# Optimization experiments

Measured on AMD Instinct MI355X. Metric: run time of the kernel, lower is better.

Reference implementation:

```python
import jax, jax.numpy as jnp
import numpy as np

N, E, D, ED = 50000, 800000, 64, 2


def setup_inputs() -> dict:
    key = jax.random.key(0)
    ks = jax.random.split(key, 16)
    inp = {
        "h": jax.random.normal(ks[0], (N, D), jnp.float32),
        "coord": jax.random.normal(ks[1], (N, 3), jnp.float32),
        "edge_index": jax.random.randint(ks[2], (2, E), 0, N, jnp.int32),
        "edge_attr": jax.random.normal(ks[3], (E, ED), jnp.float32),
        # edge_mlp: Linear(2D+1+ED -> D), Linear(D -> D)
        "W_e1": jax.random.normal(ks[4], (2 * D + 1 + ED, D), jnp.float32) * 0.08,
        "b_e1": jnp.zeros((D,), jnp.float32),
        "W_e2": jax.random.normal(ks[5], (D, D), jnp.float32) * 0.12,
        "b_e2": jnp.zeros((D,), jnp.float32),
        # node_mlp: Linear(D+D -> D), Linear(D -> D)
        "W_n1": jax.random.normal(ks[6], (2 * D, D), jnp.float32) * 0.08,
        "b_n1": jnp.zeros((D,), jnp.float32),
        "W_n2": jax.random.normal(ks[7], (D, D), jnp.float32) * 0.12,
        "b_n2": jnp.zeros((D,), jnp.float32),
        # coord_mlp: Linear(D -> D), Linear(D -> 1, bias=False, xavier gain 0.001)
        "W_c1": jax.random.normal(ks[8], (D, D), jnp.float32) * 0.12,
        "b_c1": jnp.zeros((D,), jnp.float32),
        "W_c2": jax.random.normal(ks[9], (D, 1), jnp.float32) * 1e-3,
    }
    return inp


def reference(h, coord, edge_index, edge_attr,
              W_e1, b_e1, W_e2, b_e2,
              W_n1, b_n1, W_n2, b_n2,
              W_c1, b_c1, W_c2):
    row, col = edge_index[0], edge_index[1]
    n_nodes = h.shape[0]

    # coord2radial
    coord_diff = coord[row] - coord[col]                       # [E,3]
    radial = jnp.sum(coord_diff * coord_diff, axis=-1, keepdims=True)  # [E,1]

    # edge_model
    e_in = jnp.concatenate([h[row], h[col], radial, edge_attr], axis=-1)  # [E, 2D+1+ED]
    e = jax.nn.silu(e_in @ W_e1 + b_e1)
    edge_feat = jax.nn.silu(e @ W_e2 + b_e2)                   # [E,D]

    # coord_model: trans = coord_diff * coord_mlp(edge_feat), clamp, segment mean
    scale = jax.nn.silu(edge_feat @ W_c1 + b_c1) @ W_c2        # [E,1]
    trans = jnp.clip(coord_diff * scale, -100.0, 100.0)        # [E,3]
    agg_c = jax.ops.segment_sum(trans, row, num_segments=n_nodes)       # [N,3]
    cnt = jax.ops.segment_sum(jnp.ones((trans.shape[0],), trans.dtype), row,
                              num_segments=n_nodes)            # [N]
    coord_out = coord + agg_c / jnp.clip(cnt, 1.0, None)[:, None]  # coords_weight=1.0

    # node_model: segment sum of edge_feat by row, node MLP, residual
    agg_h = jax.ops.segment_sum(edge_feat, row, num_segments=n_nodes)   # [N,D]
    n_in = jnp.concatenate([h, agg_h], axis=-1)                # [N,2D]
    h_out = h + (jax.nn.silu(n_in @ W_n1 + b_n1) @ W_n2 + b_n2)

    return (h_out, coord_out)
```

## Files before the change

### kernel.cpp

```cpp
#include <hip/hip_runtime.h>

#define DD 64
#define NTE 512
#define SLOTMAX 64

using s8v   = __attribute__((ext_vector_type(8))) short;
using f32x4 = __attribute__((ext_vector_type(4))) float;

typedef unsigned int   uint_t;
typedef unsigned short ushort_t;

union U8 { s8v v; uint_t u[4]; };

__device__ __forceinline__ float silu_f(float x) {
    return x / (1.0f + __expf(-x));
}
__device__ __forceinline__ float clamp100(float x) {
    return fminf(fmaxf(x, -100.0f), 100.0f);
}
__device__ __forceinline__ unsigned short f2bf(float x) {
    unsigned int u = __float_as_uint(x);
    return (unsigned short)((u + 0x7FFFu + ((u >> 16) & 1u)) >> 16);
}
__device__ __forceinline__ uint_t cvt_pk_bf16(float lo, float hi) {
    uint_t r;
    asm("v_cvt_pk_bf16_f32 %0, %1, %2" : "=v"(r) : "v"(lo), "v"(hi));
    return r;
}

#define WAVE_FENCE() do { asm volatile("s_waitcnt lgkmcnt(0)" ::: "memory"); \
                          __builtin_amdgcn_sched_barrier(0); } while (0)

__global__ __launch_bounds__(256) void prep_all(
    const float* __restrict__ h,
    const float* __restrict__ We1, const float* __restrict__ We2,
    const float* __restrict__ Wc1,
    const float* __restrict__ Wn1, const float* __restrict__ Wn2,
    const float* __restrict__ be1, const float* __restrict__ be2,
    const float* __restrict__ bc1,
    const int*   __restrict__ ei,
    ushort_t* __restrict__ hbf,
    ushort_t* __restrict__ wf,
    int* __restrict__ cnt_i,
    int* __restrict__ slots,
    int E, int total8, int histBlocks, int hbfBlocks)
{
    const int b = blockIdx.x;
    if (b < histBlocks) {
        const int e = b * 256 + threadIdx.x;
        if (e < E) {
            const int r = ei[e];
            const int s = atomicAdd(&cnt_i[r], 1);
            if (s < SLOTMAX) slots[(size_t)r * SLOTMAX + s] = e;
        }
    } else if (b < histBlocks + hbfBlocks) {
        const int t = (b - histBlocks) * 256 + threadIdx.x;
        if (t < total8) {
            const float4 v0 = ((const float4*)h)[t * 2 + 0];
            const float4 v1 = ((const float4*)h)[t * 2 + 1];
            uint4 o;
            o.x = (uint_t)f2bf(v0.x) | ((uint_t)f2bf(v0.y) << 16);
            o.y = (uint_t)f2bf(v0.z) | ((uint_t)f2bf(v0.w) << 16);
            o.z = (uint_t)f2bf(v1.x) | ((uint_t)f2bf(v1.y) << 16);
            o.w = (uint_t)f2bf(v1.z) | ((uint_t)f2bf(v1.w) << 16);
            ((uint4*)hbf)[t] = o;
        }
    } else {
        const int t = (b - histBlocks - hbfBlocks) * 256 + threadIdx.x;
        if (t >= 32768) return;
        if (t < 28672) {
            const int j    = t & 7;
            const int lane = (t >> 3) & 63;
            const int n0   = (t >> 9) & 3;
            const int k0   = (t >> 11) & 1;
            const int mat  = t >> 12;
            const int g    = lane >> 4;
            int k;
            if (mat == 2 || mat == 3) k = 16 * (2 * k0 + (j >> 2)) + 4 * g + (j & 3);
            else                      k = k0 * 32 + g * 8 + j;
            const int n = n0 * 16 + (lane & 15);
            float v;
            if      (mat == 0) v = We1[(size_t)k * 64 + n];
            else if (mat == 1) v = We1[(size_t)(64 + k) * 64 + n];
            else if (mat == 2) v = We2[(size_t)k * 64 + n];
            else if (mat == 3) v = Wc1[(size_t)k * 64 + n];
            else if (mat == 4) v = Wn1[(size_t)k * 64 + n];
            else if (mat == 5) v = Wn1[(size_t)(64 + k) * 64 + n];
            else               v = Wn2[(size_t)k * 64 + n];
            wf[t] = f2bf(v);
        } else {
            const int t2   = t - 28672;
            const int j    = t2 & 7;
            const int lane = (t2 >> 3) & 63;
            const int n0   = (t2 >> 9) & 3;
            const int xm   = (t2 >> 11) & 1;
            const int k = 8 * (lane >> 4) + j;
            const int m = n0 * 16 + (lane & 15);
            float v = 0.0f;
            if (xm == 0) {
                if      (k == 0) v = We1[(size_t)128 * 64 + m];
                else if (k == 1) v = We1[(size_t)129 * 64 + m];
                else if (k == 2) v = We1[(size_t)130 * 64 + m];
                else if (k == 3) v = be1[m];
            } else {
                if      (k == 0) v = be2[m];
                else if (k == 1) v = bc1[m];
            }
            wf[t] = f2bf(v);
        }
    }
}

__global__ __launch_bounds__(NTE, 4) void egcl_edge(
    const ushort_t* __restrict__ hbf,
    const ushort_t* __restrict__ wfG,
    const float* __restrict__ coord,
    const int*   __restrict__ ei,
    const float* __restrict__ ea,
    const float* __restrict__ Wc2,
    const int* __restrict__ cnt_i,
    const int* __restrict__ slots,
    ushort_t* __restrict__ aggbf,
    float* __restrict__ coord_out,
    int N, int E, int totalWaves)
{
    __shared__ ushort_t fragLDS[20480];

    const int tid = threadIdx.x;
    #pragma unroll
    for (int i = 0; i < 4; ++i)
        ((uint4*)fragLDS)[tid + i * 512] = ((const uint4*)wfG)[tid + i * 512];
    ((uint4*)fragLDS)[2048 + tid] = ((const uint4*)wfG)[3584 + tid];
    __syncthreads();

    const int wid  = tid >> 6;
    const int lane = tid & 63;
    const int l15  = lane & 15;
    const int g    = lane >> 4;

#define LD_W(mat, k0, m0) \
    (*(const s8v*)(fragLDS + ((((mat)*2 + (k0))*4 + (m0)) * 512) + lane * 8))
#define LD_X7(m0) (*(const s8v*)(fragLDS + 16384 + (m0) * 512 + lane * 8))
#define LD_XB(m0) (*(const s8v*)(fragLDS + 18432 + (m0) * 512 + lane * 8))

    float wc2_c[4][4];
    #pragma unroll
    for (int m0 = 0; m0 < 4; ++m0)
        #pragma unroll
        for (int j = 0; j < 4; ++j)
            wc2_c[m0][j] = Wc2[m0 * 16 + 4 * g + j];

    U8 b2f, bcf;
    b2f.u[0] = 0x00003F80u; b2f.u[1] = 0; b2f.u[2] = 0; b2f.u[3] = 0;
    bcf.u[0] = 0x3F800000u; bcf.u[1] = 0; bcf.u[2] = 0; bcf.u[3] = 0;

    const f32x4 zero4 = {0.f, 0.f, 0.f, 0.f};

    int n = blockIdx.x * 8 + wid;
    int pdeg = 0, pslot = 0;
    if (n < N) {
        pdeg  = cnt_i[n];
        pslot = slots[(size_t)n * SLOTMAX + l15];
    }

    for (; n < N; n += totalWaves) {
        const int deg   = pdeg;
        const int slot0 = pslot;
        const int nn = n + totalWaves;
        if (nn < N) {
            pdeg  = cnt_i[nn];
            pslot = slots[(size_t)nn * SLOTMAX + l15];
        }

        const int effdeg = deg < SLOTMAX ? deg : SLOTMAX;
        const float cnx = coord[n * 3 + 0];
        const float cny = coord[n * 3 + 1];
        const float cnz = coord[n * 3 + 2];
        const int slot0_l0 = __shfl(slot0, lane & 48, 64);

        const ushort_t* hn = hbf + (size_t)n * 64;
        const s8v bn0 = *(const s8v*)(hn + g * 8);
        const s8v bn1 = *(const s8v*)(hn + 32 + g * 8);
        f32x4 rowacc[4];
        #pragma unroll
        for (int m0 = 0; m0 < 4; ++m0) {
            f32x4 a = zero4;
            a = __builtin_amdgcn_mfma_f32_16x16x32_bf16(LD_W(0, 0, m0), bn0, a, 0, 0, 0);
            a = __builtin_amdgcn_mfma_f32_16x16x32_bf16(LD_W(0, 1, m0), bn1, a, 0, 0, 0);
            rowacc[m0] = a;
        }

        float hsum[4][4];
        #pragma unroll
        for (int m0 = 0; m0 < 4; ++m0)
            #pragma unroll
            for (int j = 0; j < 4; ++j) hsum[m0][j] = 0.f;
        float txs = 0.f, tys = 0.f, tzs = 0.f;

        const int ntile = (effdeg + 15) >> 4;
        for (int t = 0; t < ntile; ++t) {
            const int s = t * 16 + l15;
            const bool val = (s < effdeg);
            int eL;
            if (t == 0) eL = val ? slot0 : slot0_l0;
            else        eL = slots[(size_t)n * SLOTMAX + (val ? s : 0)];

            const int ci = ei[E + eL];
            const float cx = coord[ci * 3 + 0];
            const float cy = coord[ci * 3 + 1];
            const float cz = coord[ci * 3 + 2];
            const float dx = cnx - cx, dy = cny - cy, dz = cnz - cz;
            const float radial = dx * dx + dy * dy + dz * dz;
            const float2 a2 = *(const float2*)(ea + (size_t)eL * 2);
            const ushort_t* hc = hbf + (size_t)ci * 64;
            const s8v bc0 = *(const s8v*)(hc + g * 8);
            const s8v bc1v = *(const s8v*)(hc + 32 + g * 8);

            U8 ex;
            ex.u[0] = cvt_pk_bf16(radial, a2.x);
            ex.u[1] = cvt_pk_bf16(a2.y, 1.0f);
            ex.u[2] = 0; ex.u[3] = 0;

            f32x4 c1[4];
            #pragma unroll
            for (int m0 = 0; m0 < 4; ++m0) {
                f32x4 a = rowacc[m0];
                a = __builtin_amdgcn_mfma_f32_16x16x32_bf16(LD_W(1, 0, m0), bc0,  a, 0, 0, 0);
                a = __builtin_amdgcn_mfma_f32_16x16x32_bf16(LD_W(1, 1, m0), bc1v, a, 0, 0, 0);
                a = __builtin_amdgcn_mfma_f32_16x16x32_bf16(LD_X7(m0),      ex.v, a, 0, 0, 0);
                c1[m0] = a;
            }

            U8 f2a, f2b;
            #pragma unroll
            for (int m0 = 0; m0 < 4; ++m0) {
                const float ya = silu_f(c1[m0][0]);
                const float yb = silu_f(c1[m0][1]);
                const float yc = silu_f(c1[m0][2]);
                const float yd = silu_f(c1[m0][3]);
                U8& dst = (m0 < 2) ? f2a : f2b;
                dst.u[(m0 & 1) * 2 + 0] = cvt_pk_bf16(ya, yb);
                dst.u[(m0 & 1) * 2 + 1] = cvt_pk_bf16(yc, yd);
            }

            f32x4 c2[4];
            #pragma unroll
            for (int m0 = 0; m0 < 4; ++m0) {
                f32x4 a = zero4;
                a = __builtin_amdgcn_mfma_f32_16x16x32_bf16(LD_W(2, 0, m0), f2a.v, a, 0, 0, 0);
                a = __builtin_amdgcn_mfma_f32_16x16x32_bf16(LD_W(2, 1, m0), f2b.v, a, 0, 0, 0);
                a = __builtin_amdgcn_mfma_f32_16x16x32_bf16(LD_XB(m0),      b2f.v, a, 0, 0, 0);
                c2[m0] = a;
            }

            U8 f3a, f3b;
            #pragma unroll
            for (int m0 = 0; m0 < 4; ++m0) {
                const float ya = silu_f(c2[m0][0]);
                const float yb = silu_f(c2[m0][1]);
                const float yc = silu_f(c2[m0][2]);
                const float yd = silu_f(c2[m0][3]);
                hsum[m0][0] += val ? ya : 0.f;
                hsum[m0][1] += val ? yb : 0.f;
                hsum[m0][2] += val ? yc : 0.f;
                hsum[m0][3] += val ? yd : 0.f;
                U8& dst = (m0 < 2) ? f3a : f3b;
                dst.u[(m0 & 1) * 2 + 0] = cvt_pk_bf16(ya, yb);
                dst.u[(m0 & 1) * 2 + 1] = cvt_pk_bf16(yc, yd);
            }

            float p = 0.f;
            #pragma unroll
            for (int m0 = 0; m0 < 4; ++m0) {
                f32x4 a = zero4;
                a = __builtin_amdgcn_mfma_f32_16x16x32_bf16(LD_W(3, 0, m0), f3a.v, a, 0, 0, 0);
                a = __builtin_amdgcn_mfma_f32_16x16x32_bf16(LD_W(3, 1, m0), f3b.v, a, 0, 0, 0);
                a = __builtin_amdgcn_mfma_f32_16x16x32_bf16(LD_XB(m0),      bcf.v, a, 0, 0, 0);
                #pragma unroll
                for (int j = 0; j < 4; ++j)
                    p = fmaf(silu_f(a[j]), wc2_c[m0][j], p);
            }
            p += __shfl_xor(p, 16, 64);
            p += __shfl_xor(p, 32, 64);
            const float sc = val ? p : 0.f;
            txs += clamp100(dx * sc);
            tys += clamp100(dy * sc);
            tzs += clamp100(dz * sc);
        }

        #pragma unroll
        for (int m0 = 0; m0 < 4; ++m0) {
            #pragma unroll
            for (int j = 0; j < 4; ++j) {
                float v = hsum[m0][j];
                v += __shfl_xor(v, 1, 64);
                v += __shfl_xor(v, 2, 64);
                v += __shfl_xor(v, 4, 64);
                v += __shfl_xor(v, 8, 64);
                hsum[m0][j] = v;
            }
        }
        if (l15 == 0) {
            uint_t* ab = (uint_t*)aggbf + (size_t)n * 32 + 2 * g;
            #pragma unroll
            for (int m0 = 0; m0 < 4; ++m0) {
                ab[8 * m0 + 0] = cvt_pk_bf16(hsum[m0][0], hsum[m0][1]);
                ab[8 * m0 + 1] = cvt_pk_bf16(hsum[m0][2], hsum[m0][3]);
            }
        }
        #pragma unroll
        for (int msk = 1; msk < 64; msk <<= 1) {
            txs += __shfl_xor(txs, msk, 64);
            tys += __shfl_xor(tys, msk, 64);
            tzs += __shfl_xor(tzs, msk, 64);
        }
        if (lane == 0) {
            const float inv = 0.25f / fmaxf((float)deg, 1.0f);
            coord_out[(size_t)n * 3 + 0] = cnx + txs * inv;
            coord_out[(size_t)n * 3 + 1] = cny + tys * inv;
            coord_out[(size_t)n * 3 + 2] = cnz + tzs * inv;
        }
    }
#undef LD_W
#undef LD_X7
#undef LD_XB
}

__global__ __launch_bounds__(NTE, 4) void egcl_node(
    const ushort_t* __restrict__ hbf,
    const ushort_t* __restrict__ aggbf,
    const ushort_t* __restrict__ wfG,
    const float* __restrict__ h,
    const float* __restrict__ bn1,
    const float* __restrict__ bn2,
    float* __restrict__ h_out,
    int N)
{
    __shared__ ushort_t fragLDS[12288];
    __shared__ ushort_t ldsY[8][16 * 72];

    const int tid = threadIdx.x;
    #pragma unroll
    for (int i = 0; i < 3; ++i)
        ((uint4*)fragLDS)[tid + i * 512] = ((const uint4*)(wfG + 16384))[tid + i * 512];
    __syncthreads();

    const int wid  = tid >> 6;
    const int lane = tid & 63;
    const int l15  = lane & 15;
    const int g    = lane >> 4;

#define LD_WN(mat, k0, n0) \
    (*(const s8v*)(fragLDS + ((((mat)*2 + (k0))*4 + (n0)) * 512) + lane * 8))

    float bn1_c[4], bn2_c[4];
    #pragma unroll
    for (int n0 = 0; n0 < 4; ++n0) {
        bn1_c[n0] = bn1[n0 * 16 + l15];
        bn2_c[n0] = bn2[n0 * 16 + l15];
    }

    const int wg = blockIdx.x * 8 + wid;
    const int nb = wg * 16;
    if (nb >= N) return;

    const int nod  = nb + l15;
    const int nodL = nod < N ? nod : N - 1;
    const ushort_t* hrow = hbf   + (size_t)nodL * 64;
    const ushort_t* arow = aggbf + (size_t)nodL * 64;
    const s8v aH0 = *(const s8v*)(hrow + g * 8);
    const s8v aH1 = *(const s8v*)(hrow + 32 + g * 8);
    const s8v aG0 = *(const s8v*)(arow + g * 8);
    const s8v aG1 = *(const s8v*)(arow + 32 + g * 8);

    ushort_t* yw = ldsY[wid];
    #pragma unroll
    for (int n0 = 0; n0 < 4; ++n0) {
        f32x4 a = {0.f, 0.f, 0.f, 0.f};
        a = __builtin_amdgcn_mfma_f32_16x16x32_bf16(aH0, LD_WN(0, 0, n0), a, 0, 0, 0);
        a = __builtin_amdgcn_mfma_f32_16x16x32_bf16(aH1, LD_WN(0, 1, n0), a, 0, 0, 0);
        a = __builtin_amdgcn_mfma_f32_16x16x32_bf16(aG0, LD_WN(1, 0, n0), a, 0, 0, 0);
        a = __builtin_amdgcn_mfma_f32_16x16x32_bf16(aG1, LD_WN(1, 1, n0), a, 0, 0, 0);
        #pragma unroll
        for (int jj = 0; jj < 4; ++jj)
            yw[(g * 4 + jj) * 72 + n0 * 16 + l15] = f2bf(silu_f(a[jj] + bn1_c[n0]));
    }
    WAVE_FENCE();

    const ushort_t* yrow = yw + l15 * 72;
    const s8v b0 = *(const s8v*)(yrow + g * 8);
    const s8v b1 = *(const s8v*)(yrow + 32 + g * 8);
    #pragma unroll
    for (int n0 = 0; n0 < 4; ++n0) {
        f32x4 a = {0.f, 0.f, 0.f, 0.f};
        a = __builtin_amdgcn_mfma_f32_16x16x32_bf16(b0, LD_WN(2, 0, n0), a, 0, 0, 0);
        a = __builtin_amdgcn_mfma_f32_16x16x32_bf16(b1, LD_WN(2, 1, n0), a, 0, 0, 0);
        #pragma unroll
        for (int jj = 0; jj < 4; ++jj) {
            const int m = nb + g * 4 + jj;
            if (m < N) {
                const size_t idx = (size_t)m * 64 + n0 * 16 + l15;
                h_out[idx] = h[idx] + (a[jj] + bn2_c[n0]);
            }
        }
    }
#undef LD_WN
}

extern "C" void kernel_launch(void* const* d_in, const int* in_sizes, int n_in,
                              void* d_out, int out_size, void* d_ws, size_t ws_size,
                              hipStream_t stream) {
    const float* h     = (const float*)d_in[0];
    const float* coord = (const float*)d_in[1];
    const int*   ei    = (const int*)  d_in[2];
    const float* ea    = (const float*)d_in[3];
    const float* We1   = (const float*)d_in[4];
    const float* be1   = (const float*)d_in[5];
    const float* We2   = (const float*)d_in[6];
    const float* be2   = (const float*)d_in[7];
    const float* Wn1   = (const float*)d_in[8];
    const float* bn1   = (const float*)d_in[9];
    const float* Wn2   = (const float*)d_in[10];
    const float* bn2   = (const float*)d_in[11];
    const float* Wc1   = (const float*)d_in[12];
    const float* bc1   = (const float*)d_in[13];
    const float* Wc2   = (const float*)d_in[14];

    const int N = in_sizes[0] / DD;
    const int E = in_sizes[3] / 2;

    float* out       = (float*)d_out;
    float* h_out     = out;
    float* coord_out = out + (size_t)N * DD;

    char* base = (char*)d_ws;
    ushort_t* hbf   = (ushort_t*)base;
    const size_t o_wf    = (size_t)N * DD * 2;
    ushort_t* wf    = (ushort_t*)(base + o_wf);
    const size_t o_agg   = o_wf + 32768 * 2;
    ushort_t* aggbf = (ushort_t*)(base + o_agg);
    const size_t o_cnt   = o_agg + (size_t)N * DD * 2;
    int* cnt_i      = (int*)(base + o_cnt);
    const size_t o_slots = o_cnt + (size_t)N * 4;
    int* slots      = (int*)(base + o_slots);

    hipMemsetAsync((void*)cnt_i, 0, (size_t)N * 4, stream);

    const int histBlocks = (E + 255) / 256;
    const int total8     = N * DD / 8;
    const int hbfBlocks  = (total8 + 255) / 256;
    const int wfBlocks   = (32768 + 255) / 256;
    prep_all<<<histBlocks + hbfBlocks + wfBlocks, 256, 0, stream>>>(
        h, We1, We2, Wc1, Wn1, Wn2, be1, be2, bc1, ei,
        hbf, wf, cnt_i, slots, E, total8, histBlocks, hbfBlocks);

    const int eblocks = 512;
    const int totalWaves = eblocks * 8;
    egcl_edge<<<eblocks, NTE, 0, stream>>>(
        hbf, wf, coord, ei, ea, Wc2,
        cnt_i, slots, aggbf, coord_out, N, E, totalWaves);

    const int nwaves  = (N + 15) / 16;
    const int nblocks = (nwaves + 7) / 8;
    egcl_node<<<nblocks, NTE, 0, stream>>>(
        hbf, aggbf, wf, h, bn1, bn2, h_out, N);
}
```

Baseline: 250.4 us.

## Store column index in slots, pad coords to float4, prefetch next slot tile

The histogram pass now stores (edge id, column node) pairs, so the edge kernel no longer needs a dependent load of edge_index to find the neighbour. Coordinates are repacked into padded float4 so each neighbour's position comes from one vector load. The next tile's slot entries are prefetched inside the loop, and the edge kernel's launch bounds and grid size are doubled to raise occupancy. The cost is a larger slots buffer, an extra prep pass, and tighter register limits under the new launch bounds, which could cause spills.

```diff
diff --git a/kernel.cpp b/kernel.cpp
--- a/kernel.cpp
+++ b/kernel.cpp
@@ -33,6 +33,7 @@
 
 __global__ __launch_bounds__(256) void prep_all(
     const float* __restrict__ h,
+    const float* __restrict__ coord,
     const float* __restrict__ We1, const float* __restrict__ We2,
     const float* __restrict__ Wc1,
     const float* __restrict__ Wn1, const float* __restrict__ Wn2,
@@ -41,9 +42,10 @@
     const int*   __restrict__ ei,
     ushort_t* __restrict__ hbf,
     ushort_t* __restrict__ wf,
+    float4* __restrict__ coord4,
     int* __restrict__ cnt_i,
-    int* __restrict__ slots,
-    int E, int total8, int histBlocks, int hbfBlocks)
+    int2* __restrict__ slots2,
+    int N, int E, int total8, int histBlocks, int hbfBlocks, int c4Blocks)
 {
     const int b = blockIdx.x;
     if (b < histBlocks) {
@@ -51,7 +53,10 @@
         if (e < E) {
             const int r = ei[e];
             const int s = atomicAdd(&cnt_i[r], 1);
-            if (s < SLOTMAX) slots[(size_t)r * SLOTMAX + s] = e;
+            if (s < SLOTMAX) {
+                int2 v; v.x = e; v.y = ei[E + e];
+                slots2[(size_t)r * SLOTMAX + s] = v;
+            }
         }
     } else if (b < histBlocks + hbfBlocks) {
         const int t = (b - histBlocks) * 256 + threadIdx.x;
@@ -65,8 +70,18 @@
             o.w = (uint_t)f2bf(v1.z) | ((uint_t)f2bf(v1.w) << 16);
             ((uint4*)hbf)[t] = o;
         }
+    } else if (b < histBlocks + hbfBlocks + c4Blocks) {
+        const int t = (b - histBlocks - hbfBlocks) * 256 + threadIdx.x;
+        if (t < N) {
+            float4 c;
+            c.x = coord[3 * t + 0];
+            c.y = coord[3 * t + 1];
+            c.z = coord[3 * t + 2];
+            c.w = 0.0f;
+            coord4[t] = c;
+        }
     } else {
-        const int t = (b - histBlocks - hbfBlocks) * 256 + threadIdx.x;
+        const int t = (b - histBlocks - hbfBlocks - c4Blocks) * 256 + threadIdx.x;
         if (t >= 32768) return;
         if (t < 28672) {
             const int j    = t & 7;
@@ -111,18 +126,17 @@
     }
 }
 
-__global__ __launch_bounds__(NTE, 4) void egcl_edge(
+__global__ __launch_bounds__(NTE, 8) void egcl_edge(
     const ushort_t* __restrict__ hbf,
     const ushort_t* __restrict__ wfG,
-    const float* __restrict__ coord,
-    const int*   __restrict__ ei,
+    const float4* __restrict__ coord4,
     const float* __restrict__ ea,
     const float* __restrict__ Wc2,
     const int* __restrict__ cnt_i,
-    const int* __restrict__ slots,
+    const int2* __restrict__ slots2,
     ushort_t* __restrict__ aggbf,
     float* __restrict__ coord_out,
-    int N, int E, int totalWaves)
+    int N, int totalWaves)
 {
     __shared__ ushort_t fragLDS[20480];
 
@@ -157,26 +171,26 @@
     const f32x4 zero4 = {0.f, 0.f, 0.f, 0.f};
 
     int n = blockIdx.x * 8 + wid;
-    int pdeg = 0, pslot = 0;
+    int pdeg = 0;
+    int2 pslot; pslot.x = 0; pslot.y = 0;
     if (n < N) {
         pdeg  = cnt_i[n];
-        pslot = slots[(size_t)n * SLOTMAX + l15];
+        pslot = slots2[(size_t)n * SLOTMAX + l15];
     }
 
     for (; n < N; n += totalWaves) {
-        const int deg   = pdeg;
-        const int slot0 = pslot;
+        const int deg    = pdeg;
+        const int2 slot0 = pslot;
         const int nn = n + totalWaves;
         if (nn < N) {
             pdeg  = cnt_i[nn];
-            pslot = slots[(size_t)nn * SLOTMAX + l15];
+            pslot = slots2[(size_t)nn * SLOTMAX + l15];
         }
 
         const int effdeg = deg < SLOTMAX ? deg : SLOTMAX;
-        const float cnx = coord[n * 3 + 0];
-        const float cny = coord[n * 3 + 1];
-        const float cnz = coord[n * 3 + 2];
-        const int slot0_l0 = __shfl(slot0, lane & 48, 64);
+        const float4 cn4 = coord4[n];
+        const int s0x = __shfl(slot0.x, lane & 48, 64);
+        const int s0y = __shfl(slot0.y, lane & 48, 64);
 
         const ushort_t* hn = hbf + (size_t)n * 64;
         const s8v bn0 = *(const s8v*)(hn + g * 8);
@@ -198,23 +212,30 @@
         float txs = 0.f, tys = 0.f, tzs = 0.f;
 
         const int ntile = (effdeg + 15) >> 4;
+        int2 slNext; slNext.x = 0; slNext.y = 0;
+
         for (int t = 0; t < ntile; ++t) {
             const int s = t * 16 + l15;
             const bool val = (s < effdeg);
-            int eL;
-            if (t == 0) eL = val ? slot0 : slot0_l0;
-            else        eL = slots[(size_t)n * SLOTMAX + (val ? s : 0)];
-
-            const int ci = ei[E + eL];
-            const float cx = coord[ci * 3 + 0];
-            const float cy = coord[ci * 3 + 1];
-            const float cz = coord[ci * 3 + 2];
-            const float dx = cnx - cx, dy = cny - cy, dz = cnz - cz;
+            const float valf = val ? 1.0f : 0.0f;
+
+            int2 sl;
+            if (t == 0) { sl.x = val ? slot0.x : s0x; sl.y = val ? slot0.y : s0y; }
+            else        sl = slNext;
+
+            if (t + 1 < ntile) {
+                const int s2 = s + 16;
+                slNext = slots2[(size_t)n * SLOTMAX + (s2 < effdeg ? s2 : 0)];
+            }
+
+            const float4 c4 = coord4[sl.y];
+            const float2 a2 = *(const float2*)(ea + 2 * (size_t)sl.x);
+            const ushort_t* hc = hbf + (size_t)sl.y * 64;
+            const s8v bc0  = *(const s8v*)(hc + g * 8);
+            const s8v bc1v = *(const s8v*)(hc + 32 + g * 8);
+
+            const float dx = cn4.x - c4.x, dy = cn4.y - c4.y, dz = cn4.z - c4.z;
             const float radial = dx * dx + dy * dy + dz * dz;
-            const float2 a2 = *(const float2*)(ea + (size_t)eL * 2);
-            const ushort_t* hc = hbf + (size_t)ci * 64;
-            const s8v bc0 = *(const s8v*)(hc + g * 8);
-            const s8v bc1v = *(const s8v*)(hc + 32 + g * 8);
 
             U8 ex;
             ex.u[0] = cvt_pk_bf16(radial, a2.x);
@@ -260,10 +281,10 @@
                 const float yb = silu_f(c2[m0][1]);
                 const float yc = silu_f(c2[m0][2]);
                 const float yd = silu_f(c2[m0][3]);
-                hsum[m0][0] += val ? ya : 0.f;
-                hsum[m0][1] += val ? yb : 0.f;
-                hsum[m0][2] += val ? yc : 0.f;
-                hsum[m0][3] += val ? yd : 0.f;
+                hsum[m0][0] = fmaf(ya, valf, hsum[m0][0]);
+                hsum[m0][1] = fmaf(yb, valf, hsum[m0][1]);
+                hsum[m0][2] = fmaf(yc, valf, hsum[m0][2]);
+                hsum[m0][3] = fmaf(yd, valf, hsum[m0][3]);
                 U8& dst = (m0 < 2) ? f3a : f3b;
                 dst.u[(m0 & 1) * 2 + 0] = cvt_pk_bf16(ya, yb);
                 dst.u[(m0 & 1) * 2 + 1] = cvt_pk_bf16(yc, yd);
@@ -282,7 +303,7 @@
             }
             p += __shfl_xor(p, 16, 64);
             p += __shfl_xor(p, 32, 64);
-            const float sc = val ? p : 0.f;
+            const float sc = p * valf;
             txs += clamp100(dx * sc);
             tys += clamp100(dy * sc);
             tzs += clamp100(dz * sc);
@@ -316,9 +337,9 @@
         }
         if (lane == 0) {
             const float inv = 0.25f / fmaxf((float)deg, 1.0f);
-            coord_out[(size_t)n * 3 + 0] = cnx + txs * inv;
-            coord_out[(size_t)n * 3 + 1] = cny + tys * inv;
-            coord_out[(size_t)n * 3 + 2] = cnz + tzs * inv;
+            coord_out[(size_t)n * 3 + 0] = cn4.x + txs * inv;
+            coord_out[(size_t)n * 3 + 1] = cn4.y + tys * inv;
+            coord_out[(size_t)n * 3 + 2] = cn4.z + tzs * inv;
         }
     }
 #undef LD_W
@@ -439,26 +460,30 @@
     ushort_t* wf    = (ushort_t*)(base + o_wf);
     const size_t o_agg   = o_wf + 32768 * 2;
     ushort_t* aggbf = (ushort_t*)(base + o_agg);
-    const size_t o_cnt   = o_agg + (size_t)N * DD * 2;
+    const size_t o_c4    = o_agg + (size_t)N * DD * 2;
+    float4* coord4  = (float4*)(base + o_c4);
+    const size_t o_cnt   = o_c4 + (size_t)N * 16;
     int* cnt_i      = (int*)(base + o_cnt);
     const size_t o_slots = o_cnt + (size_t)N * 4;
-    int* slots      = (int*)(base + o_slots);
+    int2* slots2    = (int2*)(base + o_slots);
 
     hipMemsetAsync((void*)cnt_i, 0, (size_t)N * 4, stream);
 
     const int histBlocks = (E + 255) / 256;
     const int total8     = N * DD / 8;
     const int hbfBlocks  = (total8 + 255) / 256;
+    const int c4Blocks   = (N + 255) / 256;
     const int wfBlocks   = (32768 + 255) / 256;
-    prep_all<<<histBlocks + hbfBlocks + wfBlocks, 256, 0, stream>>>(
-        h, We1, We2, Wc1, Wn1, Wn2, be1, be2, bc1, ei,
-        hbf, wf, cnt_i, slots, E, total8, histBlocks, hbfBlocks);
-
-    const int eblocks = 512;
+    prep_all<<<histBlocks + hbfBlocks + c4Blocks + wfBlocks, 256, 0, stream>>>(
+        h, coord, We1, We2, Wc1, Wn1, Wn2, be1, be2, bc1, ei,
+        hbf, wf, coord4, cnt_i, slots2, N, E, total8,
+        histBlocks, hbfBlocks, c4Blocks);
+
+    const int eblocks = 1024;
     const int totalWaves = eblocks * 8;
     egcl_edge<<<eblocks, NTE, 0, stream>>>(
-        hbf, wf, coord, ei, ea, Wc2,
-        cnt_i, slots, aggbf, coord_out, N, E, totalWaves);
+        hbf, wf, coord4, ea, Wc2,
+        cnt_i, slots2, aggbf, coord_out, N, totalWaves);
 
     const int nwaves  = (N + 15) / 16;
     const int nblocks = (nwaves + 7) / 8;
```

Result: slower. 451.8 us (+80.4%).
